# Optimization experiments

Measured on AMD Instinct MI355X. Metric: run time of the kernel, lower is better.

Reference implementation:

```python
import jax, jax.numpy as jnp
import numpy as np

D = 3  # interpolation dimensionality (trilinear)


def nd_corners(d):
    # corner offsets of the d-dim unit hypercube: [1, 2^d, d] int32
    xi = [jnp.arange(2, dtype=jnp.int32) for _ in range(d)]
    return jnp.stack(jnp.meshgrid(*xi, indexing='ij'), -1).reshape(1, 2 ** d, d)


def setup_inputs() -> dict:
    key = jax.random.key(0)
    k1, k2 = jax.random.split(key)
    input = jax.random.normal(k1, (16, 128, 128, 128), dtype=jnp.float32)
    # normalized coords in [-1, 1]
    coords = jax.random.uniform(k2, (1000000, 3), dtype=jnp.float32) * 2.0 - 1.0
    return {"input": input, "coords": coords}


def reference(input, coords):
    d = D
    grid_shape = jnp.asarray(input.shape[-d:], dtype=coords.dtype)  # [d]
    # _unnormalize: map [-1, 1] -> grid coords
    c = (coords + 1.0) / 2.0 * (grid_shape - 1.0)
    S = c.shape[:-1]
    c = c.reshape(-1, 1, d)                      # [N, 1, d]
    corners = nd_corners(d)                       # [1, 2^d, d]
    floor = jnp.floor(c)
    # weights_fn: |x - floor(x) + i - 1|, product over dims -> [N, 2^d]
    weights = jnp.abs(c - floor + corners.astype(c.dtype) - 1.0).prod(-1)
    # index_fn + nearest clamp
    index = floor.astype(jnp.int32) + corners     # [N, 2^d, d]
    high = jnp.asarray(input.shape[-d:], dtype=jnp.int32)
    index = jnp.clip(index, 0, high - 1)
    # gather corner values: input[..., i0, i1, i2] -> [C, N, 2^d]
    values = input[..., index[..., 0], index[..., 1], index[..., 2]]
    out = (weights * values).sum(-1)              # [C, N]
    return out.reshape(*input.shape[:-d], *S)
```

## Files before the change

### kernel.cpp

```cpp
#include <hip/hip_runtime.h>
#include <hip/hip_bf16.h>


#define GD   128
#define NCH  16
constexpr int VOX = GD * GD * GD;

__device__ __forceinline__ unsigned short f2bf_rne(float f) {
    unsigned u = __builtin_bit_cast(unsigned, f);
    u = u + 0x7fffu + ((u >> 16) & 1u);
    return (unsigned short)(u >> 16);
}

__global__ __launch_bounds__(256) void transpose_bf16_k(const float* __restrict__ in,
                                                        unsigned short* __restrict__ ws) {
    int t = blockIdx.x * 256 + threadIdx.x;
    int s = t * 4;
    float4 v[NCH];
#pragma unroll
    for (int c = 0; c < NCH; ++c)
        v[c] = *(const float4*)(in + (size_t)c * VOX + s);

    const float* vf = (const float*)v;
#pragma unroll
    for (int j = 0; j < 4; ++j) {
        unsigned p[8];
#pragma unroll
        for (int k = 0; k < 8; ++k) {
            unsigned lo = f2bf_rne(vf[(2 * k + 0) * 4 + j]);
            unsigned hi = f2bf_rne(vf[(2 * k + 1) * 4 + j]);
            p[k] = lo | (hi << 16);
        }
        uint4* o = (uint4*)(ws + (size_t)(s + j) * NCH);
        o[0] = make_uint4(p[0], p[1], p[2], p[3]);
        o[1] = make_uint4(p[4], p[5], p[6], p[7]);
    }
}

__global__ __launch_bounds__(256) void interp_bf16_k(const unsigned short* __restrict__ ws,
                                                     const float* __restrict__ coords,
                                                     float* __restrict__ out, int N) {
    int n = blockIdx.x * 256 + threadIdx.x;
    if (n >= N) return;

    float cx = (coords[3 * n + 0] + 1.0f) * 0.5f * (float)(GD - 1);
    float cy = (coords[3 * n + 1] + 1.0f) * 0.5f * (float)(GD - 1);
    float cz = (coords[3 * n + 2] + 1.0f) * 0.5f * (float)(GD - 1);

    float fx = floorf(cx), fy = floorf(cy), fz = floorf(cz);
    float tx = cx - fx, ty = cy - fy, tz = cz - fz;
    int ix = (int)fx, iy = (int)fy, iz = (int)fz;

    int ix0 = min(max(ix,     0), GD - 1), ix1 = min(max(ix + 1, 0), GD - 1);
    int iy0 = min(max(iy,     0), GD - 1), iy1 = min(max(iy + 1, 0), GD - 1);
    int iz0 = min(max(iz,     0), GD - 1), iz1 = min(max(iz + 1, 0), GD - 1);

    float wx0 = 1.0f - tx, wx1 = tx;
    float wy0 = 1.0f - ty, wy1 = ty;
    float wz0 = 1.0f - tz, wz1 = tz;

    size_t bx0 = (size_t)ix0 * (GD * GD * NCH), bx1 = (size_t)ix1 * (GD * GD * NCH);
    size_t by0 = (size_t)iy0 * (GD * NCH),      by1 = (size_t)iy1 * (GD * NCH);
    size_t bz0 = (size_t)iz0 * NCH,             bz1 = (size_t)iz1 * NCH;

    float acc[NCH];
#pragma unroll
    for (int c = 0; c < NCH; ++c) acc[c] = 0.0f;

#define CORNER(BX, BY, BZ, W)                                                  \
    {                                                                          \
        const uint4* p = (const uint4*)(ws + (BX) + (BY) + (BZ));              \
        uint4 A = p[0], B = p[1];                                              \
        unsigned u[8] = {A.x, A.y, A.z, A.w, B.x, B.y, B.z, B.w};              \
        float w = (W);                                                         \
        _Pragma("unroll")                                                      \
        for (int k = 0; k < 8; ++k) {                                          \
            float lo = __builtin_bit_cast(float, u[k] << 16);                  \
            float hi = __builtin_bit_cast(float, u[k] & 0xffff0000u);          \
            acc[2 * k + 0] += w * lo;                                          \
            acc[2 * k + 1] += w * hi;                                          \
        }                                                                      \
    }

    CORNER(bx0, by0, bz0, wx0 * wy0 * wz0)
    CORNER(bx0, by0, bz1, wx0 * wy0 * wz1)
    CORNER(bx0, by1, bz0, wx0 * wy1 * wz0)
    CORNER(bx0, by1, bz1, wx0 * wy1 * wz1)
    CORNER(bx1, by0, bz0, wx1 * wy0 * wz0)
    CORNER(bx1, by0, bz1, wx1 * wy0 * wz1)
    CORNER(bx1, by1, bz0, wx1 * wy1 * wz0)
    CORNER(bx1, by1, bz1, wx1 * wy1 * wz1)
#undef CORNER

#pragma unroll
    for (int c = 0; c < NCH; ++c)
        out[(size_t)c * N + n] = acc[c];
}

__global__ __launch_bounds__(256) void interp_direct_k(const float* __restrict__ in,
                                                       const float* __restrict__ coords,
                                                       float* __restrict__ out, int N) {
    int n = blockIdx.x * 256 + threadIdx.x;
    if (n >= N) return;

    float cx = (coords[3 * n + 0] + 1.0f) * 0.5f * (float)(GD - 1);
    float cy = (coords[3 * n + 1] + 1.0f) * 0.5f * (float)(GD - 1);
    float cz = (coords[3 * n + 2] + 1.0f) * 0.5f * (float)(GD - 1);

    float fx = floorf(cx), fy = floorf(cy), fz = floorf(cz);
    float tx = cx - fx, ty = cy - fy, tz = cz - fz;
    int ix = (int)fx, iy = (int)fy, iz = (int)fz;

    int ix0 = min(max(ix,     0), GD - 1), ix1 = min(max(ix + 1, 0), GD - 1);
    int iy0 = min(max(iy,     0), GD - 1), iy1 = min(max(iy + 1, 0), GD - 1);
    int iz0 = min(max(iz,     0), GD - 1), iz1 = min(max(iz + 1, 0), GD - 1);

    float wx0 = 1.0f - tx, wx1 = tx;
    float wy0 = 1.0f - ty, wy1 = ty;
    float wz0 = 1.0f - tz, wz1 = tz;

    int o000 = (ix0 * GD + iy0) * GD + iz0, o001 = (ix0 * GD + iy0) * GD + iz1;
    int o010 = (ix0 * GD + iy1) * GD + iz0, o011 = (ix0 * GD + iy1) * GD + iz1;
    int o100 = (ix1 * GD + iy0) * GD + iz0, o101 = (ix1 * GD + iy0) * GD + iz1;
    int o110 = (ix1 * GD + iy1) * GD + iz0, o111 = (ix1 * GD + iy1) * GD + iz1;

    float w000 = wx0 * wy0 * wz0, w001 = wx0 * wy0 * wz1;
    float w010 = wx0 * wy1 * wz0, w011 = wx0 * wy1 * wz1;
    float w100 = wx1 * wy0 * wz0, w101 = wx1 * wy0 * wz1;
    float w110 = wx1 * wy1 * wz0, w111 = wx1 * wy1 * wz1;

#pragma unroll
    for (int c = 0; c < NCH; ++c) {
        const float* g = in + (size_t)c * VOX;
        float acc = w000 * g[o000] + w001 * g[o001] + w010 * g[o010] + w011 * g[o011]
                  + w100 * g[o100] + w101 * g[o101] + w110 * g[o110] + w111 * g[o111];
        out[(size_t)c * N + n] = acc;
    }
}

extern "C" void kernel_launch(void* const* d_in, const int* in_sizes, int n_in,
                              void* d_out, int out_size, void* d_ws, size_t ws_size,
                              hipStream_t stream) {
    const float* input  = (const float*)d_in[0];
    const float* coords = (const float*)d_in[1];
    float* out = (float*)d_out;
    int N = in_sizes[1] / 3;

    size_t need = (size_t)VOX * NCH * sizeof(unsigned short);
    if (ws_size >= need) {
        transpose_bf16_k<<<VOX / 4 / 256, 256, 0, stream>>>(input, (unsigned short*)d_ws);
        interp_bf16_k<<<(N + 255) / 256, 256, 0, stream>>>((const unsigned short*)d_ws,
                                                           coords, out, N);
    } else {
        interp_direct_k<<<(N + 255) / 256, 256, 0, stream>>>(input, coords, out, N);
    }
}
```

Baseline: 355.7 us.

## Bin query points by spatial tile before gathering to improve cache locality

Adds a counting sort of the query points into 512 spatial tiles (count, scan, scatter kernels). Interpolation then runs over the sorted points so neighbouring threads gather nearby voxels. Results go to a bf16 intermediate, and an unscramble kernel writes them back in the original order. Block indices are also remapped across 8 groups, presumably to spread tiles over XCDs. This trades several extra passes, heavy atomic contention on only 512 bins, and an additional bf16 rounding of the outputs for better L2 hit rates on the 64 MB bf16 grid.

```diff
diff --git a/kernel.cpp b/kernel.cpp
--- a/kernel.cpp
+++ b/kernel.cpp
@@ -4,6 +4,8 @@
 
 #define GD   128
 #define NCH  16
+#define NTILE 8
+#define NBINS 512
 constexpr int VOX = GD * GD * GD;
 
 __device__ __forceinline__ unsigned short f2bf_rne(float f) {
@@ -37,15 +39,69 @@
     }
 }
 
-__global__ __launch_bounds__(256) void interp_bf16_k(const unsigned short* __restrict__ ws,
-                                                     const float* __restrict__ coords,
-                                                     float* __restrict__ out, int N) {
-    int n = blockIdx.x * 256 + threadIdx.x;
-    if (n >= N) return;
-
-    float cx = (coords[3 * n + 0] + 1.0f) * 0.5f * (float)(GD - 1);
-    float cy = (coords[3 * n + 1] + 1.0f) * 0.5f * (float)(GD - 1);
-    float cz = (coords[3 * n + 2] + 1.0f) * 0.5f * (float)(GD - 1);
+__device__ __forceinline__ void grid_coords(const float* __restrict__ coords, int n,
+                                            float& cx, float& cy, float& cz) {
+    cx = (coords[3 * n + 0] + 1.0f) * 0.5f * (float)(GD - 1);
+    cy = (coords[3 * n + 1] + 1.0f) * 0.5f * (float)(GD - 1);
+    cz = (coords[3 * n + 2] + 1.0f) * 0.5f * (float)(GD - 1);
+}
+
+__device__ __forceinline__ int tile_of(float cx, float cy, float cz) {
+    int ix = min(max((int)floorf(cx), 0), GD - 1);
+    int iy = min(max((int)floorf(cy), 0), GD - 1);
+    int iz = min(max((int)floorf(cz), 0), GD - 1);
+    return ((ix >> 4) * NTILE + (iy >> 4)) * NTILE + (iz >> 4);
+}
+
+__global__ void zero_bins_k(unsigned* __restrict__ bins) {
+    bins[threadIdx.x] = 0u;
+}
+
+__global__ __launch_bounds__(256) void count_k(const float* __restrict__ coords,
+                                               unsigned* __restrict__ bins, int N) {
+    int n = blockIdx.x * 256 + threadIdx.x;
+    if (n >= N) return;
+    float cx, cy, cz; grid_coords(coords, n, cx, cy, cz);
+    atomicAdd(&bins[tile_of(cx, cy, cz)], 1u);
+}
+
+__global__ void scan_k(const unsigned* __restrict__ bins, unsigned* __restrict__ offs) {
+    __shared__ unsigned s[NBINS];
+    int t = threadIdx.x;
+    s[t] = bins[t];
+    __syncthreads();
+    unsigned orig = s[t];
+    for (int d = 1; d < NBINS; d <<= 1) {
+        unsigned add = (t >= d) ? s[t - d] : 0u;
+        __syncthreads();
+        s[t] += add;
+        __syncthreads();
+    }
+    offs[t] = s[t] - orig;
+}
+
+__global__ __launch_bounds__(256) void scatter_k(const float* __restrict__ coords,
+                                                 unsigned* __restrict__ offs,
+                                                 float4* __restrict__ B,
+                                                 unsigned* __restrict__ inv, int N) {
+    int n = blockIdx.x * 256 + threadIdx.x;
+    if (n >= N) return;
+    float cx, cy, cz; grid_coords(coords, n, cx, cy, cz);
+    unsigned pos = atomicAdd(&offs[tile_of(cx, cy, cz)], 1u);
+    B[pos] = make_float4(cx, cy, cz, 0.0f);
+    inv[n] = pos;
+}
+
+__global__ __launch_bounds__(256) void interp_sorted_k(const unsigned short* __restrict__ ws,
+                                                       const float4* __restrict__ B,
+                                                       unsigned short* __restrict__ C,
+                                                       int N, int K) {
+    int l = (blockIdx.x & 7) * K + (blockIdx.x >> 3);
+    int i = l * 256 + threadIdx.x;
+    if (i >= N) return;
+
+    float4 r = B[i];
+    float cx = r.x, cy = r.y, cz = r.z;
 
     float fx = floorf(cx), fy = floorf(cy), fz = floorf(cz);
     float tx = cx - fx, ty = cy - fy, tz = cz - fz;
@@ -70,8 +126,8 @@
 #define CORNER(BX, BY, BZ, W)                                                  \
     {                                                                          \
         const uint4* p = (const uint4*)(ws + (BX) + (BY) + (BZ));              \
-        uint4 A = p[0], B = p[1];                                              \
-        unsigned u[8] = {A.x, A.y, A.z, A.w, B.x, B.y, B.z, B.w};              \
+        uint4 A0 = p[0], A1 = p[1];                                            \
+        unsigned u[8] = {A0.x, A0.y, A0.z, A0.w, A1.x, A1.y, A1.z, A1.w};      \
         float w = (W);                                                         \
         _Pragma("unroll")                                                      \
         for (int k = 0; k < 8; ++k) {                                          \
@@ -92,9 +148,32 @@
     CORNER(bx1, by1, bz1, wx1 * wy1 * wz1)
 #undef CORNER
 
-#pragma unroll
-    for (int c = 0; c < NCH; ++c)
-        out[(size_t)c * N + n] = acc[c];
+    unsigned q[8];
+#pragma unroll
+    for (int k = 0; k < 8; ++k) {
+        unsigned lo = f2bf_rne(acc[2 * k + 0]);
+        unsigned hi = f2bf_rne(acc[2 * k + 1]);
+        q[k] = lo | (hi << 16);
+    }
+    uint4* o = (uint4*)(C + (size_t)i * NCH);
+    o[0] = make_uint4(q[0], q[1], q[2], q[3]);
+    o[1] = make_uint4(q[4], q[5], q[6], q[7]);
+}
+
+__global__ __launch_bounds__(256) void unscramble_k(const unsigned short* __restrict__ C,
+                                                    const unsigned* __restrict__ inv,
+                                                    float* __restrict__ out, int N) {
+    int n = blockIdx.x * 256 + threadIdx.x;
+    if (n >= N) return;
+    unsigned pos = inv[n];
+    const uint4* p = (const uint4*)(C + (size_t)pos * NCH);
+    uint4 A0 = p[0], A1 = p[1];
+    unsigned u[8] = {A0.x, A0.y, A0.z, A0.w, A1.x, A1.y, A1.z, A1.w};
+#pragma unroll
+    for (int k = 0; k < 8; ++k) {
+        out[(size_t)(2 * k + 0) * N + n] = __builtin_bit_cast(float, u[k] << 16);
+        out[(size_t)(2 * k + 1) * N + n] = __builtin_bit_cast(float, u[k] & 0xffff0000u);
+    }
 }
 
 __global__ __launch_bounds__(256) void interp_direct_k(const float* __restrict__ in,
@@ -102,33 +181,22 @@
                                                        float* __restrict__ out, int N) {
     int n = blockIdx.x * 256 + threadIdx.x;
     if (n >= N) return;
-
-    float cx = (coords[3 * n + 0] + 1.0f) * 0.5f * (float)(GD - 1);
-    float cy = (coords[3 * n + 1] + 1.0f) * 0.5f * (float)(GD - 1);
-    float cz = (coords[3 * n + 2] + 1.0f) * 0.5f * (float)(GD - 1);
-
+    float cx, cy, cz; grid_coords(coords, n, cx, cy, cz);
     float fx = floorf(cx), fy = floorf(cy), fz = floorf(cz);
     float tx = cx - fx, ty = cy - fy, tz = cz - fz;
     int ix = (int)fx, iy = (int)fy, iz = (int)fz;
-
-    int ix0 = min(max(ix,     0), GD - 1), ix1 = min(max(ix + 1, 0), GD - 1);
-    int iy0 = min(max(iy,     0), GD - 1), iy1 = min(max(iy + 1, 0), GD - 1);
-    int iz0 = min(max(iz,     0), GD - 1), iz1 = min(max(iz + 1, 0), GD - 1);
-
-    float wx0 = 1.0f - tx, wx1 = tx;
-    float wy0 = 1.0f - ty, wy1 = ty;
-    float wz0 = 1.0f - tz, wz1 = tz;
-
+    int ix0 = min(max(ix, 0), GD - 1), ix1 = min(max(ix + 1, 0), GD - 1);
+    int iy0 = min(max(iy, 0), GD - 1), iy1 = min(max(iy + 1, 0), GD - 1);
+    int iz0 = min(max(iz, 0), GD - 1), iz1 = min(max(iz + 1, 0), GD - 1);
+    float wx0 = 1.0f - tx, wx1 = tx, wy0 = 1.0f - ty, wy1 = ty, wz0 = 1.0f - tz, wz1 = tz;
     int o000 = (ix0 * GD + iy0) * GD + iz0, o001 = (ix0 * GD + iy0) * GD + iz1;
     int o010 = (ix0 * GD + iy1) * GD + iz0, o011 = (ix0 * GD + iy1) * GD + iz1;
     int o100 = (ix1 * GD + iy0) * GD + iz0, o101 = (ix1 * GD + iy0) * GD + iz1;
     int o110 = (ix1 * GD + iy1) * GD + iz0, o111 = (ix1 * GD + iy1) * GD + iz1;
-
     float w000 = wx0 * wy0 * wz0, w001 = wx0 * wy0 * wz1;
     float w010 = wx0 * wy1 * wz0, w011 = wx0 * wy1 * wz1;
     float w100 = wx1 * wy0 * wz0, w101 = wx1 * wy0 * wz1;
     float w110 = wx1 * wy1 * wz0, w111 = wx1 * wy1 * wz1;
-
 #pragma unroll
     for (int c = 0; c < NCH; ++c) {
         const float* g = in + (size_t)c * VOX;
@@ -146,12 +214,34 @@
     float* out = (float*)d_out;
     int N = in_sizes[1] / 3;
 
-    size_t need = (size_t)VOX * NCH * sizeof(unsigned short);
+    char* w = (char*)d_ws;
+    size_t offA    = 0;
+    size_t offB    = offA + (size_t)VOX * NCH * 2;
+    size_t offInv  = offB + (size_t)N * 16;
+    size_t offC    = offInv + (size_t)N * 4;
+    size_t offBins = offC + (size_t)N * NCH * 2;
+    size_t need    = offBins + 2 * NBINS * 4;
+
+    int nb = (N + 255) / 256;
+
     if (ws_size >= need) {
-        transpose_bf16_k<<<VOX / 4 / 256, 256, 0, stream>>>(input, (unsigned short*)d_ws);
-        interp_bf16_k<<<(N + 255) / 256, 256, 0, stream>>>((const unsigned short*)d_ws,
-                                                           coords, out, N);
+        unsigned short* A   = (unsigned short*)(w + offA);
+        float4*         B   = (float4*)(w + offB);
+        unsigned*       inv = (unsigned*)(w + offInv);
+        unsigned short* C   = (unsigned short*)(w + offC);
+        unsigned*       bins = (unsigned*)(w + offBins);
+        unsigned*       offs = bins + NBINS;
+        int K  = (nb + 7) / 8;
+        int nb8 = 8 * K;
+
+        transpose_bf16_k<<<VOX / 4 / 256, 256, 0, stream>>>(input, A);
+        zero_bins_k<<<1, NBINS, 0, stream>>>(bins);
+        count_k<<<nb, 256, 0, stream>>>(coords, bins, N);
+        scan_k<<<1, NBINS, 0, stream>>>(bins, offs);
+        scatter_k<<<nb, 256, 0, stream>>>(coords, offs, B, inv, N);
+        interp_sorted_k<<<nb8, 256, 0, stream>>>(A, B, C, N, K);
+        unscramble_k<<<nb, 256, 0, stream>>>(C, inv, out, N);
     } else {
-        interp_direct_k<<<(N + 255) / 256, 256, 0, stream>>>(input, coords, out, N);
-    }
-}
+        interp_direct_k<<<nb, 256, 0, stream>>>(input, coords, out, N);
+    }
+}
```

New measurement: 919.5 us. 158% more time.

## Store z-neighbor pairs contiguously so each xy corner is one 64-byte load

Applied to the files above, without the earlier changes.

The transpose kernel now writes, for each voxel, the bf16 channel vector of that voxel and of its z+1 neighbour (clamped at the edge) side by side, 64 bytes per voxel. The interpolation kernel then gathers four 64-byte chunks instead of eight 32-byte chunks and blends along z in registers. This cuts the number of random gather transactions, but doubles the workspace to 128 MB and makes the transpose read each input element twice and write twice as much.

```diff
diff --git a/kernel.cpp b/kernel.cpp
--- a/kernel.cpp
+++ b/kernel.cpp
@@ -12,32 +12,30 @@
     return (unsigned short)(u >> 16);
 }
 
-__global__ __launch_bounds__(256) void transpose_bf16_k(const float* __restrict__ in,
-                                                        unsigned short* __restrict__ ws) {
-    int t = blockIdx.x * 256 + threadIdx.x;
-    int s = t * 4;
-    float4 v[NCH];
+__global__ __launch_bounds__(256) void transpose_pair_k(const float* __restrict__ in,
+                                                        uint4* __restrict__ ws) {
+    int s = blockIdx.x * 256 + threadIdx.x;
+    int z = s & (GD - 1);
+    int s1 = s + (z < GD - 1 ? 1 : 0);
+
+    unsigned pz0[8], pz1[8];
 #pragma unroll
-    for (int c = 0; c < NCH; ++c)
-        v[c] = *(const float4*)(in + (size_t)c * VOX + s);
-
-    const float* vf = (const float*)v;
-#pragma unroll
-    for (int j = 0; j < 4; ++j) {
-        unsigned p[8];
-#pragma unroll
-        for (int k = 0; k < 8; ++k) {
-            unsigned lo = f2bf_rne(vf[(2 * k + 0) * 4 + j]);
-            unsigned hi = f2bf_rne(vf[(2 * k + 1) * 4 + j]);
-            p[k] = lo | (hi << 16);
-        }
-        uint4* o = (uint4*)(ws + (size_t)(s + j) * NCH);
-        o[0] = make_uint4(p[0], p[1], p[2], p[3]);
-        o[1] = make_uint4(p[4], p[5], p[6], p[7]);
+    for (int k = 0; k < 8; ++k) {
+        float a0 = in[(size_t)(2 * k + 0) * VOX + s];
+        float a1 = in[(size_t)(2 * k + 1) * VOX + s];
+        float b0 = in[(size_t)(2 * k + 0) * VOX + s1];
+        float b1 = in[(size_t)(2 * k + 1) * VOX + s1];
+        pz0[k] = (unsigned)f2bf_rne(a0) | ((unsigned)f2bf_rne(a1) << 16);
+        pz1[k] = (unsigned)f2bf_rne(b0) | ((unsigned)f2bf_rne(b1) << 16);
     }
+    uint4* o = ws + (size_t)s * 4;
+    o[0] = make_uint4(pz0[0], pz0[1], pz0[2], pz0[3]);
+    o[1] = make_uint4(pz0[4], pz0[5], pz0[6], pz0[7]);
+    o[2] = make_uint4(pz1[0], pz1[1], pz1[2], pz1[3]);
+    o[3] = make_uint4(pz1[4], pz1[5], pz1[6], pz1[7]);
 }
 
-__global__ __launch_bounds__(256) void interp_bf16_k(const unsigned short* __restrict__ ws,
+__global__ __launch_bounds__(256) void interp_pair_k(const uint4* __restrict__ ws,
                                                      const float* __restrict__ coords,
                                                      float* __restrict__ out, int N) {
     int n = blockIdx.x * 256 + threadIdx.x;
@@ -53,43 +51,43 @@
 
     int ix0 = min(max(ix,     0), GD - 1), ix1 = min(max(ix + 1, 0), GD - 1);
     int iy0 = min(max(iy,     0), GD - 1), iy1 = min(max(iy + 1, 0), GD - 1);
-    int iz0 = min(max(iz,     0), GD - 1), iz1 = min(max(iz + 1, 0), GD - 1);
+    int iz0 = min(max(iz,     0), GD - 1);
 
     float wx0 = 1.0f - tx, wx1 = tx;
     float wy0 = 1.0f - ty, wy1 = ty;
     float wz0 = 1.0f - tz, wz1 = tz;
 
-    size_t bx0 = (size_t)ix0 * (GD * GD * NCH), bx1 = (size_t)ix1 * (GD * GD * NCH);
-    size_t by0 = (size_t)iy0 * (GD * NCH),      by1 = (size_t)iy1 * (GD * NCH);
-    size_t bz0 = (size_t)iz0 * NCH,             bz1 = (size_t)iz1 * NCH;
+    size_t b00 = ((size_t)(ix0 * GD + iy0) * GD + iz0) * 4;
+    size_t b01 = ((size_t)(ix0 * GD + iy1) * GD + iz0) * 4;
+    size_t b10 = ((size_t)(ix1 * GD + iy0) * GD + iz0) * 4;
+    size_t b11 = ((size_t)(ix1 * GD + iy1) * GD + iz0) * 4;
 
     float acc[NCH];
 #pragma unroll
     for (int c = 0; c < NCH; ++c) acc[c] = 0.0f;
 
-#define CORNER(BX, BY, BZ, W)                                                  \
+#define CORNER(BASE, WXY)                                                      \
     {                                                                          \
-        const uint4* p = (const uint4*)(ws + (BX) + (BY) + (BZ));              \
-        uint4 A = p[0], B = p[1];                                              \
-        unsigned u[8] = {A.x, A.y, A.z, A.w, B.x, B.y, B.z, B.w};              \
-        float w = (W);                                                         \
+        const uint4* p = ws + (BASE);                                          \
+        uint4 q0 = p[0], q1 = p[1], q2 = p[2], q3 = p[3];                      \
+        unsigned u0[8] = {q0.x, q0.y, q0.z, q0.w, q1.x, q1.y, q1.z, q1.w};     \
+        unsigned u1[8] = {q2.x, q2.y, q2.z, q2.w, q3.x, q3.y, q3.z, q3.w};     \
+        float wxy = (WXY);                                                     \
         _Pragma("unroll")                                                      \
         for (int k = 0; k < 8; ++k) {                                          \
-            float lo = __builtin_bit_cast(float, u[k] << 16);                  \
-            float hi = __builtin_bit_cast(float, u[k] & 0xffff0000u);          \
-            acc[2 * k + 0] += w * lo;                                          \
-            acc[2 * k + 1] += w * hi;                                          \
+            float z0lo = __builtin_bit_cast(float, u0[k] << 16);               \
+            float z0hi = __builtin_bit_cast(float, u0[k] & 0xffff0000u);       \
+            float z1lo = __builtin_bit_cast(float, u1[k] << 16);               \
+            float z1hi = __builtin_bit_cast(float, u1[k] & 0xffff0000u);       \
+            acc[2 * k + 0] += wxy * (wz0 * z0lo + wz1 * z1lo);                 \
+            acc[2 * k + 1] += wxy * (wz0 * z0hi + wz1 * z1hi);                 \
         }                                                                      \
     }
 
-    CORNER(bx0, by0, bz0, wx0 * wy0 * wz0)
-    CORNER(bx0, by0, bz1, wx0 * wy0 * wz1)
-    CORNER(bx0, by1, bz0, wx0 * wy1 * wz0)
-    CORNER(bx0, by1, bz1, wx0 * wy1 * wz1)
-    CORNER(bx1, by0, bz0, wx1 * wy0 * wz0)
-    CORNER(bx1, by0, bz1, wx1 * wy0 * wz1)
-    CORNER(bx1, by1, bz0, wx1 * wy1 * wz0)
-    CORNER(bx1, by1, bz1, wx1 * wy1 * wz1)
+    CORNER(b00, wx0 * wy0)
+    CORNER(b01, wx0 * wy1)
+    CORNER(b10, wx1 * wy0)
+    CORNER(b11, wx1 * wy1)
 #undef CORNER
 
 #pragma unroll
@@ -102,33 +100,24 @@
                                                        float* __restrict__ out, int N) {
     int n = blockIdx.x * 256 + threadIdx.x;
     if (n >= N) return;
-
     float cx = (coords[3 * n + 0] + 1.0f) * 0.5f * (float)(GD - 1);
     float cy = (coords[3 * n + 1] + 1.0f) * 0.5f * (float)(GD - 1);
     float cz = (coords[3 * n + 2] + 1.0f) * 0.5f * (float)(GD - 1);
-
     float fx = floorf(cx), fy = floorf(cy), fz = floorf(cz);
     float tx = cx - fx, ty = cy - fy, tz = cz - fz;
     int ix = (int)fx, iy = (int)fy, iz = (int)fz;
-
-    int ix0 = min(max(ix,     0), GD - 1), ix1 = min(max(ix + 1, 0), GD - 1);
-    int iy0 = min(max(iy,     0), GD - 1), iy1 = min(max(iy + 1, 0), GD - 1);
-    int iz0 = min(max(iz,     0), GD - 1), iz1 = min(max(iz + 1, 0), GD - 1);
-
-    float wx0 = 1.0f - tx, wx1 = tx;
-    float wy0 = 1.0f - ty, wy1 = ty;
-    float wz0 = 1.0f - tz, wz1 = tz;
-
+    int ix0 = min(max(ix, 0), GD - 1), ix1 = min(max(ix + 1, 0), GD - 1);
+    int iy0 = min(max(iy, 0), GD - 1), iy1 = min(max(iy + 1, 0), GD - 1);
+    int iz0 = min(max(iz, 0), GD - 1), iz1 = min(max(iz + 1, 0), GD - 1);
+    float wx0 = 1.0f - tx, wx1 = tx, wy0 = 1.0f - ty, wy1 = ty, wz0 = 1.0f - tz, wz1 = tz;
     int o000 = (ix0 * GD + iy0) * GD + iz0, o001 = (ix0 * GD + iy0) * GD + iz1;
     int o010 = (ix0 * GD + iy1) * GD + iz0, o011 = (ix0 * GD + iy1) * GD + iz1;
     int o100 = (ix1 * GD + iy0) * GD + iz0, o101 = (ix1 * GD + iy0) * GD + iz1;
     int o110 = (ix1 * GD + iy1) * GD + iz0, o111 = (ix1 * GD + iy1) * GD + iz1;
-
     float w000 = wx0 * wy0 * wz0, w001 = wx0 * wy0 * wz1;
     float w010 = wx0 * wy1 * wz0, w011 = wx0 * wy1 * wz1;
     float w100 = wx1 * wy0 * wz0, w101 = wx1 * wy0 * wz1;
     float w110 = wx1 * wy1 * wz0, w111 = wx1 * wy1 * wz1;
-
 #pragma unroll
     for (int c = 0; c < NCH; ++c) {
         const float* g = in + (size_t)c * VOX;
@@ -145,13 +134,13 @@
     const float* coords = (const float*)d_in[1];
     float* out = (float*)d_out;
     int N = in_sizes[1] / 3;
+    int nb = (N + 255) / 256;
 
-    size_t need = (size_t)VOX * NCH * sizeof(unsigned short);
+    size_t need = (size_t)VOX * 64;
     if (ws_size >= need) {
-        transpose_bf16_k<<<VOX / 4 / 256, 256, 0, stream>>>(input, (unsigned short*)d_ws);
-        interp_bf16_k<<<(N + 255) / 256, 256, 0, stream>>>((const unsigned short*)d_ws,
-                                                           coords, out, N);
+        transpose_pair_k<<<VOX / 256, 256, 0, stream>>>(input, (uint4*)d_ws);
+        interp_pair_k<<<nb, 256, 0, stream>>>((const uint4*)d_ws, coords, out, N);
     } else {
-        interp_direct_k<<<(N + 255) / 256, 256, 0, stream>>>(input, coords, out, N);
+        interp_direct_k<<<nb, 256, 0, stream>>>(input, coords, out, N);
     }
 }
```

After: 344.0 us. -3.3%, faster.
